# Performance work log

Measured on AMD Instinct MI355X. Metric: run time of the kernel, lower is better.

The kernel has to match this reference:

```python
import jax, jax.numpy as jnp
import numpy as np

B, K, D = 1024, 262144, 64

def setup_inputs() -> dict:
    key = jax.random.key(0)
    k1, k2 = jax.random.split(key)
    query_vec = jax.random.normal(k1, (B, D), dtype=jnp.float32)
    memory = jax.random.normal(k2, (K, D), dtype=jnp.float32)
    return {"query_vec": query_vec, "memory": memory, "topk": 5}

def reference(query_vec, memory, topk):
    # sim: [B, K] similarity against the full memory bank
    sim = jnp.einsum('bd,kd->bk', query_vec, memory)
    # indices of top-k most similar bank rows: [B, topk]
    _, topk_idx = jax.lax.top_k(sim, topk)
    # gather rows: [B, topk, D]
    return memory[topk_idx]
```

## Files before the change

kernel.cpp:

```cpp
#include <hip/hip_runtime.h>
#include <stdint.h>

typedef unsigned long long u64;
typedef __attribute__((ext_vector_type(8))) short short8;
typedef __attribute__((ext_vector_type(4))) float f32x4;

#define KROWS  262144
#define DDIM   64
#define NQ     1024
#define NC     256
#define CHUNK  (KROWS / NC)
#define SUB    128
#define NSUB   (CHUNK / SUB)
#define KC_PER 4
#define BIAS   128.0f
#define SIMMASK 0xFFFFFC00u

__device__ __forceinline__ uint32_t ord32(float f) {
    uint32_t u = __float_as_uint(f);
    return (u & 0x80000000u) ? ~u : (u | 0x80000000u);
}
__device__ __forceinline__ uint32_t maxu(uint32_t a, uint32_t b) { return a > b ? a : b; }
__device__ __forceinline__ uint32_t minu(uint32_t a, uint32_t b) { return a < b ? a : b; }
__device__ __forceinline__ void fold2(uint32_t& t0, uint32_t& t1, uint32_t k) {
    t1 = maxu(t1, minu(t0, k));
    t0 = maxu(t0, k);
}
__device__ __forceinline__ void fold4(uint32_t (&t)[4], uint32_t k) {
    uint32_t n1 = maxu(t[1], minu(t[0], k));
    uint32_t n2 = maxu(t[2], minu(t[1], k));
    uint32_t n3 = maxu(t[3], minu(t[2], k));
    t[0] = maxu(t[0], k);
    t[1] = n1; t[2] = n2; t[3] = n3;
}
__device__ __forceinline__ uint32_t cvtpk(float a, float b) {
    uint32_t r;
    asm("v_cvt_pk_bf16_f32 %0, %1, %2" : "=v"(r) : "v"(a), "v"(b));
    return r;
}

__global__ __launch_bounds__(512)
__attribute__((amdgpu_waves_per_eu(4, 8)))
void p1(const float* __restrict__ Qg,
        const float* __restrict__ Mf,
        uint32_t* __restrict__ wsK) {
    __shared__ __align__(16) uint16_t stage[2 * 8192];
    const int t = threadIdx.x;
    const int lane = t & 63;
    const int w = t >> 6;
    const int quad = lane >> 4;
    const int m = lane & 15;
    const int qcol = blockIdx.x;
    const int chunk = blockIdx.y;
    const int qBase = qcol * 256 + w * 32;
    const int rowChunk = chunk * CHUNK;

    short8 afr[2][2];
    #pragma unroll
    for (int qt = 0; qt < 2; ++qt)
        #pragma unroll
        for (int kh = 0; kh < 2; ++kh) {
            const float* qp = Qg + (size_t)(qBase + qt * 16 + m) * DDIM + quad * 8 + kh * 32;
            const float4 f0 = ((const float4*)qp)[0];
            const float4 f1 = ((const float4*)qp)[1];
            union { short8 s; uint32_t u[4]; } cv;
            cv.u[0] = cvtpk(f0.x, f0.y);
            cv.u[1] = cvtpk(f0.z, f0.w);
            cv.u[2] = cvtpk(f1.x, f1.y);
            cv.u[3] = cvtpk(f1.z, f1.w);
            afr[qt][kh] = cv.s;
        }
    const f32x4 bias = {BIAS, BIAS, BIAS, BIAS};

    uint32_t tA[8], tB[8];
    #pragma unroll
    for (int li = 0; li < 8; ++li) { tA[li] = 0u; tB[li] = 0u; }

    const int sr0 = t >> 3;
    const int sc0 = (t & 7) ^ (sr0 & 7);
    auto stage_sub = [&](int sb, int buf) {
        const float* base = Mf + (size_t)(rowChunk + sb * SUB) * DDIM + sr0 * DDIM + sc0 * 8;
        const float4 a0 = ((const float4*)base)[0];
        const float4 a1 = ((const float4*)base)[1];
        const float4 b0 = ((const float4*)(base + 64 * DDIM))[0];
        const float4 b1 = ((const float4*)(base + 64 * DDIM))[1];
        uint16_t* bp = stage + buf * 8192;
        uint4 w0, w1;
        w0.x = cvtpk(a0.x, a0.y); w0.y = cvtpk(a0.z, a0.w);
        w0.z = cvtpk(a1.x, a1.y); w0.w = cvtpk(a1.z, a1.w);
        w1.x = cvtpk(b0.x, b0.y); w1.y = cvtpk(b0.z, b0.w);
        w1.z = cvtpk(b1.x, b1.y); w1.w = cvtpk(b1.z, b1.w);
        *(uint4*)(bp + (size_t)t * 8) = w0;
        *(uint4*)(bp + (size_t)(t + 512) * 8) = w1;
    };

    stage_sub(0, 0);
    #pragma unroll 2
    for (int sb = 0; sb < NSUB; ++sb) {
        __syncthreads();
        if (sb + 1 < NSUB) stage_sub(sb + 1, (sb + 1) & 1);
        const uint16_t* bufp = stage + (sb & 1) * 8192;
        const uint32_t pb = (uint32_t)m + (uint32_t)sb * 128u;
        #pragma unroll
        for (int rt = 0; rt < 8; ++rt) {
            const int r = rt * 16 + m;
            const short8 v0 = *(const short8*)(bufp + r * 64 + ((quad       ^ (m & 7)) * 8));
            const short8 v1 = *(const short8*)(bufp + r * 64 + (((quad + 4) ^ (m & 7)) * 8));
            f32x4 c0, c1;
            c0 = __builtin_amdgcn_mfma_f32_16x16x32_bf16(afr[0][0], v0, bias, 0, 0, 0);
            c0 = __builtin_amdgcn_mfma_f32_16x16x32_bf16(afr[0][1], v1, c0,   0, 0, 0);
            c1 = __builtin_amdgcn_mfma_f32_16x16x32_bf16(afr[1][0], v0, bias, 0, 0, 0);
            c1 = __builtin_amdgcn_mfma_f32_16x16x32_bf16(afr[1][1], v1, c1,   0, 0, 0);
            const uint32_t posm = pb + (uint32_t)(rt * 16);
            #pragma unroll
            for (int reg = 0; reg < 4; ++reg) {
                fold2(tA[reg],     tB[reg],     (__float_as_uint(c0[reg]) & SIMMASK) | posm);
                fold2(tA[4 + reg], tB[4 + reg], (__float_as_uint(c1[reg]) & SIMMASK) | posm);
            }
        }
    }

    #pragma unroll
    for (int g = 0; g < 2; ++g) {
        uint32_t fl[4][4];
        #pragma unroll
        for (int r4 = 0; r4 < 4; ++r4) {
            fl[r4][0] = tA[g * 4 + r4]; fl[r4][1] = tB[g * 4 + r4];
            fl[r4][2] = 0u;             fl[r4][3] = 0u;
        }
        #pragma unroll
        for (int d = 1; d <= 8; d <<= 1) {
            const int nv = (d == 1) ? 2 : 4;
            #pragma unroll
            for (int r4 = 0; r4 < 4; ++r4) {
                uint32_t rm[4];
                #pragma unroll
                for (int s = 0; s < 4; ++s)
                    if (s < nv) rm[s] = __shfl_xor(fl[r4][s], d, 64);
                #pragma unroll
                for (int s = 0; s < 4; ++s)
                    if (s < nv) fold4(fl[r4], rm[s]);
            }
        }
        if (m == 0) {
            #pragma unroll
            for (int r4 = 0; r4 < 4; ++r4) {
                const int q = qBase + g * 16 + quad * 4 + r4;
                uint4 v4; v4.x = fl[r4][0]; v4.y = fl[r4][1];
                v4.z = fl[r4][2]; v4.w = fl[r4][3];
                *(uint4*)(wsK + ((size_t)chunk * NQ + (size_t)q) * KC_PER) = v4;
            }
        }
    }
}

__global__ __launch_bounds__(256) void p2(const float* __restrict__ Qg,
                                          const float* __restrict__ Mf,
                                          const uint32_t* __restrict__ wsK,
                                          float* __restrict__ out) {
    const int Q = blockIdx.x * 4 + (threadIdx.x >> 6);
    const int lane = threadIdx.x & 63;
    u64 mk[16];
    #pragma unroll
    for (int i = 0; i < 4; ++i) {
        const int c = i * 64 + lane;
        const uint4 k4 = *(const uint4*)(wsK + ((size_t)c * NQ + (size_t)Q) * KC_PER);
        const uint32_t cb = (uint32_t)c * (uint32_t)CHUNK;
        mk[i * 4 + 0] = ((u64)k4.x << 32) | (u64)(cb + (k4.x & 1023u));
        mk[i * 4 + 1] = ((u64)k4.y << 32) | (u64)(cb + (k4.y & 1023u));
        mk[i * 4 + 2] = ((u64)k4.z << 32) | (u64)(cb + (k4.z & 1023u));
        mk[i * 4 + 3] = ((u64)k4.w << 32) | (u64)(cb + (k4.w & 1023u));
    }
    uint32_t idxs[16];
    #pragma unroll
    for (int it = 0; it < 16; ++it) {
        u64 wk = mk[0];
        #pragma unroll
        for (int i2 = 1; i2 < 16; ++i2) wk = mk[i2] > wk ? mk[i2] : wk;
        #pragma unroll
        for (int off = 32; off >= 1; off >>= 1) {
            const u64 o = __shfl_xor(wk, off, 64);
            wk = o > wk ? o : wk;
        }
        #pragma unroll
        for (int i2 = 0; i2 < 16; ++i2) if (mk[i2] == wk) mk[i2] = 0;
        idxs[it] = (uint32_t)wk & (KROWS - 1u);
    }
    const float qv = Qg[(size_t)Q * DDIM + lane];
    float v[16];
    #pragma unroll
    for (int j = 0; j < 16; ++j) v[j] = Mf[(size_t)idxs[j] * DDIM + lane];
    u64 rk[16];
    #pragma unroll
    for (int j = 0; j < 16; ++j) {
        float p = qv * v[j];
        #pragma unroll
        for (int off = 32; off >= 1; off >>= 1) p += __shfl_xor(p, off, 64);
        rk[j] = ((u64)ord32(p) << 32) | (u64)(~idxs[j]);
    }
    #pragma unroll
    for (int it = 0; it < 5; ++it) {
        u64 best = rk[0];
        #pragma unroll
        for (int j = 1; j < 16; ++j) best = rk[j] > best ? rk[j] : best;
        float o = 0.f;
        #pragma unroll
        for (int j = 0; j < 16; ++j) o = (rk[j] == best) ? v[j] : o;
        out[((size_t)Q * 5 + it) * DDIM + lane] = o;
        #pragma unroll
        for (int j = 0; j < 16; ++j) rk[j] = (rk[j] == best) ? 0ull : rk[j];
    }
}

extern "C" void kernel_launch(void* const* d_in, const int* in_sizes, int n_in,
                              void* d_out, int out_size, void* d_ws, size_t ws_size,
                              hipStream_t stream) {
    const float* Qg = (const float*)d_in[0];
    const float* Mf = (const float*)d_in[1];
    float* out = (float*)d_out;
    uint32_t* wsK = (uint32_t*)d_ws;

    p1<<<dim3(4, NC), 512, 0, stream>>>(Qg, Mf, wsK);
    p2<<<NQ / 4, 256, 0, stream>>>(Qg, Mf, wsK, out);
}
```

Baseline: 174.7 us.

## Halve p1 blocks and rewrite p2 as per-query block with bitonic merge

p1 now runs 256-thread blocks covering 128 queries each, with a grid twice as wide; each thread stages four memory rows per sub-tile. p2 assigns one query per 256-thread block. Each wave merges 64 chunks' candidates with a shuffle-based bitonic top-16, rescores the candidates in fp32, and then a single wave picks the final top-5 and gathers the rows. This spreads p2's serial 16-round selection across more threads and shrinks p1's block size to improve occupancy. The cost is that each memory sub-tile is staged by twice as many blocks, and p2 now keeps 64 candidates per query instead of 16.

```diff
diff --git a/kernel.cpp b/kernel.cpp
--- a/kernel.cpp
+++ b/kernel.cpp
@@ -39,7 +39,7 @@
     return r;
 }
 
-__global__ __launch_bounds__(512)
+__global__ __launch_bounds__(256)
 __attribute__((amdgpu_waves_per_eu(4, 8)))
 void p1(const float* __restrict__ Qg,
         const float* __restrict__ Mf,
@@ -52,7 +52,7 @@
     const int m = lane & 15;
     const int qcol = blockIdx.x;
     const int chunk = blockIdx.y;
-    const int qBase = qcol * 256 + w * 32;
+    const int qBase = qcol * 128 + w * 32;
     const int rowChunk = chunk * CHUNK;
 
     short8 afr[2][2];
@@ -79,19 +79,24 @@
     const int sr0 = t >> 3;
     const int sc0 = (t & 7) ^ (sr0 & 7);
     auto stage_sub = [&](int sb, int buf) {
-        const float* base = Mf + (size_t)(rowChunk + sb * SUB) * DDIM + sr0 * DDIM + sc0 * 8;
-        const float4 a0 = ((const float4*)base)[0];
-        const float4 a1 = ((const float4*)base)[1];
-        const float4 b0 = ((const float4*)(base + 64 * DDIM))[0];
-        const float4 b1 = ((const float4*)(base + 64 * DDIM))[1];
+        const float* base = Mf + (size_t)(rowChunk + sb * SUB + sr0) * DDIM + sc0 * 8;
+        float4 f[8];
+        #pragma unroll
+        for (int k = 0; k < 4; ++k) {
+            const float4* p = (const float4*)(base + (size_t)k * 32 * DDIM);
+            f[2 * k]     = p[0];
+            f[2 * k + 1] = p[1];
+        }
         uint16_t* bp = stage + buf * 8192;
-        uint4 w0, w1;
-        w0.x = cvtpk(a0.x, a0.y); w0.y = cvtpk(a0.z, a0.w);
-        w0.z = cvtpk(a1.x, a1.y); w0.w = cvtpk(a1.z, a1.w);
-        w1.x = cvtpk(b0.x, b0.y); w1.y = cvtpk(b0.z, b0.w);
-        w1.z = cvtpk(b1.x, b1.y); w1.w = cvtpk(b1.z, b1.w);
-        *(uint4*)(bp + (size_t)t * 8) = w0;
-        *(uint4*)(bp + (size_t)(t + 512) * 8) = w1;
+        #pragma unroll
+        for (int k = 0; k < 4; ++k) {
+            uint4 wv;
+            wv.x = cvtpk(f[2 * k].x,     f[2 * k].y);
+            wv.y = cvtpk(f[2 * k].z,     f[2 * k].w);
+            wv.z = cvtpk(f[2 * k + 1].x, f[2 * k + 1].y);
+            wv.w = cvtpk(f[2 * k + 1].z, f[2 * k + 1].w);
+            *(uint4*)(bp + (size_t)(t + 256 * k) * 8) = wv;
+        }
     };
 
     stage_sub(0, 0);
@@ -158,57 +163,85 @@
                                           const float* __restrict__ Mf,
                                           const uint32_t* __restrict__ wsK,
                                           float* __restrict__ out) {
-    const int Q = blockIdx.x * 4 + (threadIdx.x >> 6);
-    const int lane = threadIdx.x & 63;
-    u64 mk[16];
-    #pragma unroll
-    for (int i = 0; i < 4; ++i) {
-        const int c = i * 64 + lane;
-        const uint4 k4 = *(const uint4*)(wsK + ((size_t)c * NQ + (size_t)Q) * KC_PER);
-        const uint32_t cb = (uint32_t)c * (uint32_t)CHUNK;
-        mk[i * 4 + 0] = ((u64)k4.x << 32) | (u64)(cb + (k4.x & 1023u));
-        mk[i * 4 + 1] = ((u64)k4.y << 32) | (u64)(cb + (k4.y & 1023u));
-        mk[i * 4 + 2] = ((u64)k4.z << 32) | (u64)(cb + (k4.z & 1023u));
-        mk[i * 4 + 3] = ((u64)k4.w << 32) | (u64)(cb + (k4.w & 1023u));
-    }
-    uint32_t idxs[16];
-    #pragma unroll
-    for (int it = 0; it < 16; ++it) {
-        u64 wk = mk[0];
-        #pragma unroll
-        for (int i2 = 1; i2 < 16; ++i2) wk = mk[i2] > wk ? mk[i2] : wk;
-        #pragma unroll
-        for (int off = 32; off >= 1; off >>= 1) {
-            const u64 o = __shfl_xor(wk, off, 64);
-            wk = o > wk ? o : wk;
-        }
-        #pragma unroll
-        for (int i2 = 0; i2 < 16; ++i2) if (mk[i2] == wk) mk[i2] = 0;
-        idxs[it] = (uint32_t)wk & (KROWS - 1u);
-    }
+    __shared__ uint32_t candRow[64];
+    __shared__ u64 candScore[64];
+    const int Q = blockIdx.x;
+    const int t = threadIdx.x;
+    const int lane = t & 63;
+    const int w = t >> 6;
+
+    const int c = w * 64 + lane;
+    const uint4 k4 = *(const uint4*)(wsK + ((size_t)c * NQ + (size_t)Q) * KC_PER);
+    uint32_t s[16];
+    s[0] = (k4.x & SIMMASK) | ((uint32_t)lane << 2) | 0u;
+    s[1] = (k4.y & SIMMASK) | ((uint32_t)lane << 2) | 1u;
+    s[2] = (k4.z & SIMMASK) | ((uint32_t)lane << 2) | 2u;
+    s[3] = (k4.w & SIMMASK) | ((uint32_t)lane << 2) | 3u;
+    #pragma unroll
+    for (int i = 4; i < 16; ++i) s[i] = 0u;
+
+    #pragma unroll
+    for (int d = 1; d <= 32; d <<= 1) {
+        uint32_t r[16];
+        #pragma unroll
+        for (int i = 0; i < 16; ++i) r[i] = __shfl_xor(s[i], d, 64);
+        uint32_t mm[16];
+        #pragma unroll
+        for (int i = 0; i < 16; ++i) mm[i] = maxu(s[i], r[15 - i]);
+        #pragma unroll
+        for (int dd = 8; dd >= 1; dd >>= 1) {
+            #pragma unroll
+            for (int i = 0; i < 16; ++i) {
+                if ((i & dd) == 0) {
+                    const uint32_t hi = maxu(mm[i], mm[i + dd]);
+                    const uint32_t lo = minu(mm[i], mm[i + dd]);
+                    mm[i] = hi; mm[i + dd] = lo;
+                }
+            }
+        }
+        #pragma unroll
+        for (int i = 0; i < 16; ++i) s[i] = mm[i];
+    }
+
+    uint32_t ck = s[0];
+    #pragma unroll
+    for (int j = 1; j < 16; ++j) ck = (lane == j) ? s[j] : ck;
+    if (lane < 16) {
+        const int srcLane = (int)((ck >> 2) & 63u);
+        const int jj = (int)(ck & 3u);
+        const int c2 = w * 64 + srcLane;
+        const uint32_t raw = wsK[((size_t)c2 * NQ + (size_t)Q) * KC_PER + jj];
+        candRow[w * 16 + lane] = (uint32_t)c2 * (uint32_t)CHUNK + (raw & 1023u);
+    }
+    __syncthreads();
+
     const float qv = Qg[(size_t)Q * DDIM + lane];
-    float v[16];
-    #pragma unroll
-    for (int j = 0; j < 16; ++j) v[j] = Mf[(size_t)idxs[j] * DDIM + lane];
-    u64 rk[16];
     #pragma unroll
     for (int j = 0; j < 16; ++j) {
-        float p = qv * v[j];
+        const uint32_t grow = candRow[w * 16 + j];
+        const float v = Mf[(size_t)grow * DDIM + lane];
+        float p = qv * v;
         #pragma unroll
         for (int off = 32; off >= 1; off >>= 1) p += __shfl_xor(p, off, 64);
-        rk[j] = ((u64)ord32(p) << 32) | (u64)(~idxs[j]);
-    }
-    #pragma unroll
-    for (int it = 0; it < 5; ++it) {
-        u64 best = rk[0];
-        #pragma unroll
-        for (int j = 1; j < 16; ++j) best = rk[j] > best ? rk[j] : best;
-        float o = 0.f;
-        #pragma unroll
-        for (int j = 0; j < 16; ++j) o = (rk[j] == best) ? v[j] : o;
-        out[((size_t)Q * 5 + it) * DDIM + lane] = o;
-        #pragma unroll
-        for (int j = 0; j < 16; ++j) rk[j] = (rk[j] == best) ? 0ull : rk[j];
+        if (lane == 0)
+            candScore[w * 16 + j] = ((u64)ord32(p) << 32) | (u64)(~grow);
+    }
+    __syncthreads();
+
+    if (w == 0) {
+        u64 key = candScore[lane];
+        #pragma unroll
+        for (int it = 0; it < 5; ++it) {
+            u64 best = key;
+            #pragma unroll
+            for (int off = 32; off >= 1; off >>= 1) {
+                const u64 o = __shfl_xor(best, off, 64);
+                best = o > best ? o : best;
+            }
+            const uint32_t wrow = ~(uint32_t)best;
+            out[((size_t)Q * 5 + it) * DDIM + lane] = Mf[(size_t)wrow * DDIM + lane];
+            key = (key == best) ? 0ull : key;
+        }
     }
 }
 
@@ -220,6 +253,6 @@
     float* out = (float*)d_out;
     uint32_t* wsK = (uint32_t*)d_ws;
 
-    p1<<<dim3(4, NC), 512, 0, stream>>>(Qg, Mf, wsK);
-    p2<<<NQ / 4, 256, 0, stream>>>(Qg, Mf, wsK, out);
-}
+    p1<<<dim3(8, NC), 256, 0, stream>>>(Qg, Mf, wsK);
+    p2<<<NQ, 256, 0, stream>>>(Qg, Mf, wsK, out);
+}
```

Measured after the change: 199.2 us. +14.0%, slower.
